# Performance work log

Hardware: AMD Instinct MI355X
Metric: run time of the kernel (lower is better)

Reference implementation:

```python
import math
import jax, jax.numpy as jnp
import numpy as np

H = 768      # hidden_size
NH = 12      # num_attention_heads
K = 3        # attention_num branches (wid = None, 2, 4)
DIV = 5.0    # gauss_divisor = 2**(attention_num-1) + 1
SFT = 1.0    # sft_factor
WIDTHS = (None, 2.0, 4.0)
B, L = 4, 1024


def _layernorm(x, s, b, eps=1e-5):
    m = jnp.mean(x, axis=-1, keepdims=True)
    v = jnp.mean((x - m) ** 2, axis=-1, keepdims=True)
    return (x - m) / jnp.sqrt(v + eps) * s + b


def _log_gauss_bias(props_len, width):
    # matches generate_gauss_weight + log(clamp_min(1e-6))
    center = jnp.arange(props_len, dtype=jnp.float32) / props_len          # (L,)
    wt = jnp.maximum(jnp.float32(width), 0.01) / DIV                       # scalar
    pos = jnp.linspace(0.0, 1.0, props_len)                                # (L,)
    g = (0.3989422804014327 / wt) * jnp.exp(-(pos[None, :] - center[:, None]) ** 2 / (2.0 * wt * wt))
    g = g / jnp.max(g, axis=-1, keepdims=True)
    return jnp.log(jnp.maximum(g, 1e-6))                                   # (L, L)


def _attn(qx, kx, vx, Wq, bq, Wk, bk, Wv, bv, bias, mask):
    Bn, Lq, D = qx.shape
    dh = D // NH
    q = (qx @ Wq + bq).reshape(Bn, Lq, NH, dh)
    k = (kx @ Wk + bk).reshape(Bn, kx.shape[1], NH, dh)
    v = (vx @ Wv + bv).reshape(Bn, vx.shape[1], NH, dh)
    s = jnp.einsum('bqhd,bkhd->bhqk', q, k) / math.sqrt(dh)
    if bias is not None:
        s = s + bias[None, None]                  # cached Gaussian log-bias
    if mask is not None:
        s = s + (1.0 - mask)[:, None, None, :] * (-10000.0)
    p = jax.nn.softmax(s, axis=-1)
    return jnp.einsum('bhqk,bkhd->bqhd', p, v).reshape(Bn, Lq, D)


def _block(x, mask, Wq, bq, Wk, bk, Wv, bv, W1, b1, W2, b2, n1s, n1b, n2s, n2b, bias):
    a = _attn(x, x, x, Wq, bq, Wk, bk, Wv, bv, bias, mask)
    x = _layernorm(x + a, n1s, n1b)
    h = jax.nn.relu(x @ W1 + b1) @ W2 + b2
    return _layernorm(x + h, n2s, n2b)


def setup_inputs():
    key = jax.random.key(0)
    ks = iter(jax.random.split(key, 64))
    def p(*sh):
        return jax.random.normal(next(ks), sh, dtype=jnp.float32) * 0.02
    inp = {}
    inp['input_tensor'] = jax.random.normal(next(ks), (B, L, H), dtype=jnp.float32)
    inp['attention_mask'] = jnp.ones((B, L), dtype=jnp.float32)
    for nm, sh in [('bWq', (K, H, H)), ('bWk', (K, H, H)), ('bWv', (K, H, H)),
                   ('bW1', (K, H, 4 * H)), ('bW2', (K, 4 * H, H)),
                   ('caWq', (H, H)), ('caWk', (H, H)), ('caWv', (H, H)),
                   ('caW1', (H, H)), ('caW2', (H, H)), ('Wl1', (H, H)), ('Wl2', (H, 1))]:
        inp[nm] = p(*sh)
    for nm, sh in [('bbq', (K, H)), ('bbk', (K, H)), ('bbv', (K, H)), ('bb1', (K, 4 * H)), ('bb2', (K, H)),
                   ('cabq', (H,)), ('cabk', (H,)), ('cabv', (H,)), ('cab1', (H,)), ('cab2', (H,)),
                   ('bl1', (H,)), ('bl2', (1,))]:
        inp[nm] = jnp.zeros(sh, dtype=jnp.float32)
    for nm, sh in [('bn1s', (K, H)), ('bn2s', (K, H)), ('bns', (H,)), ('can1s', (H,)), ('can2s', (H,))]:
        inp[nm] = jnp.ones(sh, dtype=jnp.float32)
    for nm, sh in [('bn1b', (K, H)), ('bn2b', (K, H)), ('bnb', (H,)), ('can1b', (H,)), ('can2b', (H,))]:
        inp[nm] = jnp.zeros(sh, dtype=jnp.float32)
    return inp


def reference(input_tensor, attention_mask, bWq, bbq, bWk, bbk, bWv, bbv, bW1, bb1, bW2, bb2,
              bn1s, bn1b, bn2s, bn2b, bns, bnb,
              caWq, cabq, caWk, cabk, caWv, cabv, caW1, cab1, caW2, cab2,
              can1s, can1b, can2s, can2b, Wl1, bl1, Wl2, bl2):
    Bn, Ln, _ = input_tensor.shape
    mask = attention_mask
    biases = [None if w is None else _log_gauss_bias(Ln, w) for w in WIDTHS]
    outs = []
    for i in range(K):
        o = _block(input_tensor, mask,
                   bWq[i], bbq[i], bWk[i], bbk[i], bWv[i], bbv[i],
                   bW1[i], bb1[i], bW2[i], bb2[i],
                   bn1s[i], bn1b[i], bn2s[i], bn2b[i], biases[i])
        outs.append(_layernorm(o, bns, bnb))
    oo = jnp.stack(outs, axis=-1)                                   # (B, L, H, K)
    valid = mask                                                    # (B, L)
    denom = jnp.maximum(valid.sum(axis=1, keepdims=True), 1.0)      # (B, 1)
    mean_token = (oo.mean(-1) * valid[:, :, None]).sum(axis=1, keepdims=True) / denom[:, :, None]  # (B,1,H)
    selected = mean_token  # weight_token=None, mode='global' -> global_token = mean_token
    branch_feat = jnp.transpose(oo, (0, 3, 1, 2)).reshape(Bn * K, Ln, H)
    query_token = jnp.repeat(selected, K, axis=0)                   # (B*K, 1, H)
    branch_mask = jnp.repeat(mask, K, axis=0)                       # (B*K, L)
    # CrossAttention (wid=None, FFN d_ff = H)
    a = _attn(query_token, branch_feat, branch_feat, caWq, cabq, caWk, cabk, caWv, cabv, None, branch_mask)
    q = _layernorm(query_token + a, can1s, can1b)
    t = jax.nn.relu(q @ caW1 + cab1) @ caW2 + cab2
    q = _layernorm(q + t, can2s, can2b)                             # (B*K, 1, H)
    w = q.reshape(Bn, K, H)
    w = jax.nn.relu(w @ Wl1 + bl1)
    w = (w @ Wl2 + bl2)[..., 0]                                     # (B, K)
    w = jax.nn.softmax(w / SFT, axis=-1)
    return (oo * w[:, None, None, :]).sum(axis=-1)                  # (B, L, H)
```

## Files before the change

### kernel.cpp

```cpp
#include <hip/hip_runtime.h>
#include <hip/hip_bf16.h>
#include <cstdint>
#include <cmath>

typedef __hip_bfloat16 bf16;
typedef __attribute__((ext_vector_type(8))) __bf16 bf16x8;
typedef __attribute__((ext_vector_type(4))) float f32x4;

#define NE2C ((size_t)4096 * 768)
#define WSQC ((size_t)768 * 768)

__device__ inline float ldv(const void* __restrict__ p, size_t i, bool b){
  return b ? __bfloat162float(((const bf16*)p)[i]) : ((const float*)p)[i];
}

__device__ inline float wave_sum(float v){
  #pragma unroll
  for (int o = 1; o < 64; o <<= 1) v += __shfl_xor(v, o, 64);
  return v;
}
__device__ inline float wave_max(float v){
  #pragma unroll
  for (int o = 1; o < 64; o <<= 1) v = fmaxf(v, __shfl_xor(v, o, 64));
  return v;
}

__device__ __forceinline__ void gload_lds16(const __bf16* g, __bf16* l){
  __builtin_amdgcn_global_load_lds(
      (const __attribute__((address_space(1))) uint32_t*)g,
      (__attribute__((address_space(3))) uint32_t*)l,
      16, 0, 0);
}

__global__ __launch_bounds__(256) void flagmask_kernel(const void* __restrict__ bns,
    const void* __restrict__ mask, int* __restrict__ flagp){
  const bool isb = (((const uint32_t*)bns)[0] != 0x3F800000u);
  int t = threadIdx.x;
  int ok = 1;
  for (int j = t; j < 4096; j += 256) ok &= (ldv(mask, (size_t)j, isb) == 1.0f) ? 1 : 0;
  __shared__ int allok;
  if (t == 0) { allok = 1; flagp[0] = isb ? 1 : 0; }
  __syncthreads();
  if (!ok) atomicAnd(&allok, 0);
  __syncthreads();
  if (t == 0) flagp[1] = allok;
}

__global__ __launch_bounds__(256) void cvtb_kernel(const void* __restrict__ in, __bf16* __restrict__ out,
                                                   int n, const int* __restrict__ flagp){
  const bool isb = flagp[0] != 0;
  int i = blockIdx.x * 256 + threadIdx.x;
  if (i < n) out[i] = (__bf16)ldv(in, i, isb);
}

__global__ __launch_bounds__(256) void transpose_kernel(const void* __restrict__ in, size_t in_off, size_t in_zstride,
    __bf16* __restrict__ out, size_t out_off, size_t out_zstride, int K, int N, const int* __restrict__ flagp)
{
  const bool isb = flagp[0] != 0;
  const int z = blockIdx.z;
  const size_t ioff = in_off + (size_t)z * in_zstride;
  __bf16* op = out + out_off + (size_t)z * out_zstride;
  const int n0 = blockIdx.x * 64, k0 = blockIdx.y * 64;
  __shared__ __bf16 T[64][65];
  const int cr = threadIdx.x >> 6, cc = threadIdx.x & 63;
  #pragma unroll
  for (int it = 0; it < 16; ++it) {
    int r = it * 4 + cr;
    T[r][cc] = (__bf16)ldv(in, ioff + (size_t)(k0 + r) * N + (n0 + cc), isb);
  }
  __syncthreads();
  #pragma unroll
  for (int it = 0; it < 16; ++it) {
    int r = it * 4 + cr;
    op[(size_t)(n0 + r) * K + (k0 + cc)] = T[cc][r];
  }
}

__global__ __launch_bounds__(256) void wqkvtrans_kernel(const void* __restrict__ bWq,
    const void* __restrict__ bWk, const void* __restrict__ bWv,
    __bf16* __restrict__ out, const int* __restrict__ flagp)
{
  const bool isb = flagp[0] != 0;
  const int z = blockIdx.z;
  const int br = z / 3, m = z % 3;
  const void* in = (m == 0) ? bWq : ((m == 1) ? bWk : bWv);
  const size_t ioff = (size_t)br * WSQC;
  __bf16* op = out + (size_t)z * WSQC;
  const int n0 = blockIdx.x * 64, k0 = blockIdx.y * 64;
  __shared__ __bf16 T[64][65];
  const int cr = threadIdx.x >> 6, cc = threadIdx.x & 63;
  #pragma unroll
  for (int it = 0; it < 16; ++it) {
    int r = it * 4 + cr;
    T[r][cc] = (__bf16)ldv(in, ioff + (size_t)(k0 + r) * 768 + (n0 + cc), isb);
  }
  __syncthreads();
  #pragma unroll
  for (int it = 0; it < 16; ++it) {
    int r = it * 4 + cr;
    op[(size_t)(n0 + r) * 768 + (k0 + cc)] = T[cc][r];
  }
}

__global__ __launch_bounds__(256) void vtrans_kernel(const __bf16* __restrict__ Rb, __bf16* __restrict__ VT)
{
  const int z = blockIdx.z;
  const int br = z >> 2, b = z & 3;
  const __bf16* src = Rb + (size_t)(br * 3 + 2) * NE2C;
  __bf16* dst = VT + (size_t)z * 786432;
  const int c0 = blockIdx.x * 64, k0 = blockIdx.y * 64;
  __shared__ __bf16 T[64][65];
  const int cr = threadIdx.x >> 6, cc = threadIdx.x & 63;
  #pragma unroll
  for (int it = 0; it < 16; ++it) {
    int k = it * 4 + cr;
    T[k][cc] = src[((size_t)(b * 1024 + k0 + k)) * 768 + c0 + cc];
  }
  __syncthreads();
  #pragma unroll
  for (int it = 0; it < 16; ++it) {
    int c = it * 4 + cr;
    dst[(size_t)(c0 + c) * 1024 + k0 + cc] = T[cc][c];
  }
}

__global__ __launch_bounds__(256) void biaspack_kernel(const void* bbq, const void* bbk, const void* bbv,
    const void* bb1, const void* bb2, const void* cabk, const void* cabv,
    float* __restrict__ pool, const int* __restrict__ flagp)
{
  const bool isb = flagp[0] != 0;
  int idx = blockIdx.x * 256 + threadIdx.x;
  if (idx >= 19968) return;
  float v;
  if (idx < 6912) {
    int i = idx / 2304, rem = idx % 2304;
    int m = rem / 768, c = rem % 768;
    const void* src = (m == 0) ? bbq : ((m == 1) ? bbk : bbv);
    v = ldv(src, (size_t)i * 768 + c, isb);
  } else if (idx < 16128) v = ldv(bb1, idx - 6912, isb);
  else if (idx < 18432)   v = ldv(bb2, idx - 16128, isb);
  else if (idx < 19200)   v = ldv(cabk, idx - 18432, isb);
  else                    v = ldv(cabv, idx - 19200, isb);
  pool[idx] = v;
}

__global__ __launch_bounds__(256) void gaussbias_kernel(float* __restrict__ gb)
{
  const int br = blockIdx.x >> 10;
  const int q  = blockIdx.x & 1023;
  const float inv2wt2 = (br == 0) ? 3.125f : 0.78125f;
  const float c2 = inv2wt2 * 1.4426950408889634f;
  const float cq = (float)q * (1.f / 1024.f);
  const float kst = roundf(cq * 1023.f);
  const float dd = kst * (1.f / 1023.f) - cq;
  const float dmin = dd * dd;
  float* row = gb + (size_t)br * 1048576 + (size_t)q * 1024;
  for (int o = threadIdx.x; o < 1024; o += 256) {
    int cb = o >> 6, rem = o & 63, rr = rem >> 2, t = rem & 3;
    int k = cb * 64 + t * 16 + rr;
    float d2 = (float)k * (1.f / 1023.f) - cq;
    row[o] = fmaxf((dmin - d2 * d2) * c2, -19.9315686f);
  }
}

template<int TAG>
__global__ __launch_bounds__(256) void gemm_mfma_kernel(
    const __bf16* __restrict__ A, size_t a_zstride,
    const __bf16* __restrict__ WT, const float* __restrict__ biasp,
    __bf16* __restrict__ C, int M, int N, int K, int relu)
{
  const int gx = gridDim.x, gy = gridDim.y;
  const int tot = gx * gy * gridDim.z;
  int p = (blockIdx.z * gy + blockIdx.y) * gx + blockIdx.x;
  int wg = (p & 7) * (tot >> 3) + (p >> 3);
  const int z = wg / (gx * gy);
  int rem = wg - z * gx * gy;
  const int m0 = (rem / gx) * 128, n0 = (rem % gx) * 128;

  A  += (size_t)z * a_zstride;
  WT += (size_t)z * (size_t)N * K;
  biasp += (size_t)z * N;
  C  += (size_t)z * (size_t)M * N;
  const int tid = threadIdx.x, w = tid >> 6, lane = tid & 63;
  const int quad = lane >> 4, r16 = lane & 15;
  const int wr = w >> 1, wc = w & 1;
  __shared__ __align__(16) __bf16 As[128 * 32];
  __shared__ __align__(16) __bf16 Bs[128 * 32];
  f32x4 acc[4][4];
  #pragma unroll
  for (int i = 0; i < 4; ++i)
    #pragma unroll
    for (int j = 0; j < 4; ++j) acc[i][j] = (f32x4){0.f, 0.f, 0.f, 0.f};

  const int srow = tid >> 2;
  const int scc  = (tid & 3) * 8;

  for (int k0 = 0; k0 < K; k0 += 32) {
    __syncthreads();
    #pragma unroll
    for (int it = 0; it < 2; ++it) {
      int row = it * 64 + srow;
      const __bf16* gA = A  + (size_t)(m0 + row) * K + k0 + scc;
      const __bf16* gB = WT + (size_t)(n0 + row) * K + k0 + scc;
      __bf16* lA = &As[(it * 256 + w * 64) * 8];
      __bf16* lB = &Bs[(it * 256 + w * 64) * 8];
      gload_lds16(gA, lA);
      gload_lds16(gB, lB);
    }
    __syncthreads();
    bf16x8 af[4], bf[4];
    #pragma unroll
    for (int mt = 0; mt < 4; ++mt) af[mt] = *(const bf16x8*)&As[(wr * 64 + mt * 16 + r16) * 32 + quad * 8];
    #pragma unroll
    for (int nt = 0; nt < 4; ++nt) bf[nt] = *(const bf16x8*)&Bs[(wc * 64 + nt * 16 + r16) * 32 + quad * 8];
    #pragma unroll
    for (int mt = 0; mt < 4; ++mt)
      #pragma unroll
      for (int nt = 0; nt < 4; ++nt)
        acc[mt][nt] = __builtin_amdgcn_mfma_f32_16x16x32_bf16(af[mt], bf[nt], acc[mt][nt], 0, 0, 0);
  }
  #pragma unroll
  for (int nt = 0; nt < 4; ++nt) {
    int col = n0 + wc * 64 + nt * 16 + r16;
    float bv = biasp[col];
    #pragma unroll
    for (int mt = 0; mt < 4; ++mt) {
      int rowb = m0 + wr * 64 + mt * 16 + quad * 4;
      #pragma unroll
      for (int reg = 0; reg < 4; ++reg) {
        float v = acc[mt][nt][reg] + bv;
        if (relu) v = fmaxf(v, 0.f);
        C[(size_t)(rowb + reg) * N + col] = (__bf16)v;
      }
    }
  }
}

__global__ __launch_bounds__(256) void gemm_ffn2_kernel(
    const __bf16* __restrict__ Hb, const __bf16* __restrict__ WT2,
    const float* __restrict__ biasp, __bf16* __restrict__ C0, __bf16* __restrict__ C1)
{
  const int gx = gridDim.x, gy = gridDim.y;
  const int tot = gx * gy * gridDim.z;
  int p = (blockIdx.z * gy + blockIdx.y) * gx + blockIdx.x;
  int wg = (p & 7) * (tot >> 3) + (p >> 3);
  const int z = wg / (gx * gy);
  int rem = wg - z * gx * gy;
  const int m0 = (rem / gx) * 128, n0 = (rem % gx) * 128;

  const int brn = z >> 1, half = z & 1;
  const __bf16* A  = Hb  + (size_t)brn * 4 * NE2C + half * 1536;
  const __bf16* WT = WT2 + (size_t)brn * 768 * 3072 + half * 1536;
  const float* bp = biasp + (size_t)brn * 768;
  __bf16* C = (half ? C1 : C0) + (size_t)brn * NE2C;
  const int tid = threadIdx.x, w = tid >> 6, lane = tid & 63;
  const int quad = lane >> 4, r16 = lane & 15;
  const int wr = w >> 1, wc = w & 1;
  __shared__ __align__(16) __bf16 As[128 * 32];
  __shared__ __align__(16) __bf16 Bs[128 * 32];
  f32x4 acc[4][4];
  #pragma unroll
  for (int i = 0; i < 4; ++i)
    #pragma unroll
    for (int j = 0; j < 4; ++j) acc[i][j] = (f32x4){0.f, 0.f, 0.f, 0.f};

  const int srow = tid >> 2;
  const int scc  = (tid & 3) * 8;

  for (int k0 = 0; k0 < 1536; k0 += 32) {
    __syncthreads();
    #pragma unroll
    for (int it = 0; it < 2; ++it) {
      int row = it * 64 + srow;
      const __bf16* gA = A  + (size_t)(m0 + row) * 3072 + k0 + scc;
      const __bf16* gB = WT + (size_t)(n0 + row) * 3072 + k0 + scc;
      gload_lds16(gA, &As[(it * 256 + w * 64) * 8]);
      gload_lds16(gB, &Bs[(it * 256 + w * 64) * 8]);
    }
    __syncthreads();
    bf16x8 af[4], bf[4];
    #pragma unroll
    for (int mt = 0; mt < 4; ++mt) af[mt] = *(const bf16x8*)&As[(wr * 64 + mt * 16 + r16) * 32 + quad * 8];
    #pragma unroll
    for (int nt = 0; nt < 4; ++nt) bf[nt] = *(const bf16x8*)&Bs[(wc * 64 + nt * 16 + r16) * 32 + quad * 8];
    #pragma unroll
    for (int mt = 0; mt < 4; ++mt)
      #pragma unroll
      for (int nt = 0; nt < 4; ++nt)
        acc[mt][nt] = __builtin_amdgcn_mfma_f32_16x16x32_bf16(af[mt], bf[nt], acc[mt][nt], 0, 0, 0);
  }
  #pragma unroll
  for (int nt = 0; nt < 4; ++nt) {
    int col = n0 + wc * 64 + nt * 16 + r16;
    float bv = half ? 0.f : bp[col];
    #pragma unroll
    for (int mt = 0; mt < 4; ++mt) {
      int rowb = m0 + wr * 64 + mt * 16 + quad * 4;
      #pragma unroll
      for (int reg = 0; reg < 4; ++reg)
        C[(size_t)(rowb + reg) * 768 + col] = (__bf16)(acc[mt][nt][reg] + bv);
    }
  }
}

__global__ __launch_bounds__(256) void gemm_small_kernel(const float* __restrict__ A, const void* __restrict__ W,
    size_t woff, const void* __restrict__ bias, size_t boff, float* __restrict__ C,
    int N, int K, int relu, const int* __restrict__ flagp)
{
  const bool isb = flagp[0] != 0;
  const int row = blockIdx.y;
  const int c = blockIdx.x * 64 + (threadIdx.x & 63);
  const int ks = threadIdx.x >> 6;
  const int klen = K >> 2;
  const float* ar = A + (size_t)row * K + ks * klen;
  const size_t wbase = woff + (size_t)ks * klen * N + c;
  float acc = 0.f;
  #pragma unroll 4
  for (int k = 0; k < klen; ++k)
    acc += ar[k] * ldv(W, wbase + (size_t)k * N, isb);
  __shared__ float red[4][64];
  red[ks][threadIdx.x & 63] = acc;
  __syncthreads();
  if (threadIdx.x < 64) {
    float v = red[0][threadIdx.x] + red[1][threadIdx.x] + red[2][threadIdx.x] + red[3][threadIdx.x];
    v += ldv(bias, boff + c, isb);
    if (relu) v = fmaxf(v, 0.f);
    C[(size_t)row * N + c] = v;
  }
}

__global__ __launch_bounds__(512) void attn_mfma_kernel(
    const __bf16* __restrict__ QKV, const void* __restrict__ mask,
    const float* __restrict__ gbias,
    __bf16* __restrict__ Aout, const int* __restrict__ flagp)
{
  const bool isb = flagp[0] != 0;
  const bool mall = flagp[1] != 0;
  const int gx = gridDim.x, gy = gridDim.y;
  const int tot = gx * gy * gridDim.z;
  int p = (blockIdx.z * gy + blockIdx.y) * gx + blockIdx.x;
  int wg = (p & 7) * (tot >> 3) + (p >> 3);
  const int bz = wg / (gx * gy);
  int rem2 = wg - bz * gx * gy;
  const int h = rem2 / gx;
  const int qblk = rem2 % gx;

  const int b = bz & 3, br = bz >> 2;
  const __bf16* Q  = QKV + (size_t)br * 3 * NE2C;
  const __bf16* Kg = Q + NE2C;
  const __bf16* VgT = QKV + 9 * NE2C + (size_t)bz * 786432;
  Aout += (size_t)br * NE2C;
  const int has_bias = br > 0;

  const int tid = threadIdx.x;
  const int w = tid >> 6, lane = tid & 63;
  const int quad = lane >> 4, r16 = lane & 15;
  const int qbase = qblk * 128 + w * 16;

  __shared__ __align__(16) __bf16 Ks[64 * 72];
  __shared__ __align__(16) __bf16 Vt[64 * 72];
  __shared__ __align__(16) __bf16 Ps[8][16 * 72];

  const __bf16* qrow = Q + ((size_t)(b * 1024 + qbase + r16)) * 768 + h * 64;
  bf16x8 aq0 = *(const bf16x8*)(qrow + quad * 8);
  bf16x8 aq1 = *(const bf16x8*)(qrow + 32 + quad * 8);

  const float* bq4[4];
  if (has_bias) {
    const float* gbb = gbias + (size_t)(br - 1) * 1048576 + r16 * 4;
    #pragma unroll
    for (int reg = 0; reg < 4; ++reg)
      bq4[reg] = gbb + (size_t)(qbase + quad * 4 + reg) * 1024;
  }

  float m_r[4], l_r[4];
  f32x4 O[4];
  #pragma unroll
  for (int n = 0; n < 4; ++n) O[n] = (f32x4){0.f, 0.f, 0.f, 0.f};
  #pragma unroll
  for (int reg = 0; reg < 4; ++reg) { m_r[reg] = -1e30f; l_r[reg] = 0.f; }

  const int sr0  = tid >> 3;
  const int sc8  = (tid & 7) * 8;
  const size_t kcol  = (size_t)h * 64 + sc8;
  const size_t bbase = (size_t)b * 1024;
  const __bf16* vbase = VgT + (size_t)(h * 64 + sr0) * 1024 + sc8;
  const int vls = sr0 * 72 + (((sc8 >> 3) ^ ((sr0 >> 3) & 7)) * 8);

  const float SCL = 0.18033688f;
  const float MBIG = 14426.9504f;
  const float THR2 = 11.5415603f;

  bf16x8 kpre, vpre;
  kpre = *(const bf16x8*)(Kg + (bbase + sr0) * 768 + kcol);
  vpre = *(const bf16x8*)(vbase);

  for (int c0 = 0; c0 < 1024; c0 += 64) {
    __syncthreads();
    *(bf16x8*)&Ks[sr0 * 72 + sc8] = kpre;
    *(bf16x8*)&Vt[vls] = vpre;
    __syncthreads();

    if (c0 + 64 < 1024) {
      kpre = *(const bf16x8*)(Kg + (bbase + c0 + 64 + sr0) * 768 + kcol);
      vpre = *(const bf16x8*)(vbase + c0 + 64);
    }

    f32x4 bv4[4];
    if (has_bias) {
      #pragma unroll
      for (int reg = 0; reg < 4; ++reg) bv4[reg] = *(const f32x4*)(bq4[reg] + c0);
    }

    float s4[4][4], p4[4][4];
    #pragma unroll
    for (int t = 0; t < 4; ++t) {
      bf16x8 b0 = *(const bf16x8*)&Ks[(t * 16 + r16) * 72 + quad * 8];
      bf16x8 b1 = *(const bf16x8*)&Ks[(t * 16 + r16) * 72 + 32 + quad * 8];
      f32x4 accq = (f32x4){0.f, 0.f, 0.f, 0.f};
      accq = __builtin_amdgcn_mfma_f32_16x16x32_bf16(aq0, b0, accq, 0, 0, 0);
      accq = __builtin_amdgcn_mfma_f32_16x16x32_bf16(aq1, b1, accq, 0, 0, 0);
      float mterm = 0.f;
      if (!mall) {
        int kk = c0 + t * 16 + r16;
        float mk = ldv(mask, (size_t)(b * 1024 + kk), isb);
        mterm = fmaf(mk, MBIG, -MBIG);
      }
      if (has_bias) {
        #pragma unroll
        for (int reg = 0; reg < 4; ++reg)
          s4[t][reg] = fmaf(accq[reg], SCL, mterm) + bv4[reg][t];
      } else {
        #pragma unroll
        for (int reg = 0; reg < 4; ++reg)
          s4[t][reg] = fmaf(accq[reg], SCL, mterm);
      }
    }
    float mlane[4];
    #pragma unroll
    for (int reg = 0; reg < 4; ++reg)
      mlane[reg] = fmaxf(fmaxf(s4[0][reg], s4[1][reg]), fmaxf(s4[2][reg], s4[3][reg]));
    bool need = (mlane[0] > m_r[0] + THR2) || (mlane[1] > m_r[1] + THR2)
             || (mlane[2] > m_r[2] + THR2) || (mlane[3] > m_r[3] + THR2);
    if (__any(need)) {
      #pragma unroll
      for (int reg = 0; reg < 4; ++reg) {
        float t0 = mlane[reg];
        #pragma unroll
        for (int off = 1; off < 16; off <<= 1) t0 = fmaxf(t0, __shfl_xor(t0, off, 64));
        float mnew = fmaxf(m_r[reg], t0);
        float alpha = exp2f(m_r[reg] - mnew);
        l_r[reg] *= alpha;
        m_r[reg] = mnew;
        #pragma unroll
        for (int n = 0; n < 4; ++n) O[n][reg] *= alpha;
      }
    }
    #pragma unroll
    for (int reg = 0; reg < 4; ++reg) {
      float rs = 0.f;
      #pragma unroll
      for (int t = 0; t < 4; ++t) { float p2 = exp2f(s4[t][reg] - m_r[reg]); p4[t][reg] = p2; rs += p2; }
      l_r[reg] += rs;
    }
    __bf16* pw = &Ps[w][0];
    #pragma unroll
    for (int t = 0; t < 4; ++t)
      #pragma unroll
      for (int reg = 0; reg < 4; ++reg)
        pw[(quad * 4 + reg) * 72 + t * 16 + r16] = (__bf16)p4[t][reg];
    bf16x8 ap0 = *(const bf16x8*)&pw[r16 * 72 + quad * 8];
    bf16x8 ap1 = *(const bf16x8*)&pw[r16 * 72 + 32 + quad * 8];
    __builtin_amdgcn_s_setprio(1);
    #pragma unroll
    for (int n = 0; n < 4; ++n) {
      int dr = n * 16 + r16;
      int sw = (dr >> 3) & 7;
      bf16x8 bv0 = *(const bf16x8*)&Vt[dr * 72 + (quad ^ sw) * 8];
      bf16x8 bv1 = *(const bf16x8*)&Vt[dr * 72 + ((quad + 4) ^ sw) * 8];
      O[n] = __builtin_amdgcn_mfma_f32_16x16x32_bf16(ap0, bv0, O[n], 0, 0, 0);
      O[n] = __builtin_amdgcn_mfma_f32_16x16x32_bf16(ap1, bv1, O[n], 0, 0, 0);
    }
    __builtin_amdgcn_s_setprio(0);
  }
  #pragma unroll
  for (int reg = 0; reg < 4; ++reg) {
    float lv = l_r[reg];
    #pragma unroll
    for (int off = 1; off < 16; off <<= 1) lv += __shfl_xor(lv, off, 64);
    l_r[reg] = lv;
  }
  #pragma unroll
  for (int n = 0; n < 4; ++n)
    #pragma unroll
    for (int reg = 0; reg < 4; ++reg) {
      int qg = qbase + quad * 4 + reg;
      Aout[((size_t)(b * 1024 + qg)) * 768 + h * 64 + n * 16 + r16] = (__bf16)(O[n][reg] / l_r[reg]);
    }
}

__global__ __launch_bounds__(256) void lnb_b_kernel(const __bf16* __restrict__ x, const __bf16* __restrict__ a,
    const void* __restrict__ sc, const void* __restrict__ bi, __bf16* __restrict__ out,
    const int* __restrict__ flagp)
{
  const bool isb = flagp[0] != 0;
  const int br = blockIdx.y;
  a   += (size_t)br * NE2C;
  out += (size_t)br * NE2C;
  const size_t so = (size_t)br * 768;
  int r = blockIdx.x;
  const __bf16* xr = x + (size_t)r * 768;
  const __bf16* ar = a + (size_t)r * 768;
  int t = threadIdx.x;
  float v[3]; float s = 0.f, ss = 0.f;
  #pragma unroll
  for (int j = 0; j < 3; j++) {
    int c = t + j * 256;
    float val = (float)xr[c] + (float)ar[c];
    v[j] = val; s += val; ss += val * val;
  }
  s = wave_sum(s); ss = wave_sum(ss);
  __shared__ float sred[8];
  __shared__ float stats[2];
  int lane = t & 63, wid = t >> 6;
  if (lane == 0) { sred[wid] = s; sred[4 + wid] = ss; }
  __syncthreads();
  if (t == 0) {
    float S = sred[0] + sred[1] + sred[2] + sred[3];
    float SS = sred[4] + sred[5] + sred[6] + sred[7];
    float mean = S * (1.f / 768.f);
    float var = fmaxf(SS * (1.f / 768.f) - mean * mean, 0.f);
    stats[0] = mean; stats[1] = rsqrtf(var + 1e-5f);
  }
  __syncthreads();
  float mean = stats[0], rstd = stats[1];
  #pragma unroll
  for (int j = 0; j < 3; j++) {
    int c = t + j * 256;
    out[(size_t)r * 768 + c] = (__bf16)((v[j] - mean) * rstd * ldv(sc, so + c, isb) + ldv(bi, so + c, isb));
  }
}

__global__ __launch_bounds__(256) void lnb2_b_kernel(const __bf16* __restrict__ x, const __bf16* __restrict__ a,
    const __bf16* __restrict__ a2,
    const void* __restrict__ sc1, const void* __restrict__ bi1,
    const void* __restrict__ sc2, const void* __restrict__ bi2,
    __bf16* __restrict__ out, const int* __restrict__ flagp)
{
  const bool isb = flagp[0] != 0;
  const int br = blockIdx.y;
  x   += (size_t)br * NE2C;
  a   += (size_t)br * NE2C;
  a2  += (size_t)br * NE2C;
  out += (size_t)br * NE2C;
  const size_t s1off = (size_t)br * 768;
  int r = blockIdx.x;
  const __bf16* xr = x + (size_t)r * 768;
  const __bf16* ar = a + (size_t)r * 768;
  const __bf16* ar2 = a2 + (size_t)r * 768;
  int t = threadIdx.x;
  int lane = t & 63, wid = t >> 6;
  __shared__ float sred[8], stats[2], sred2[8], stats2[2];

  float v[3]; float s = 0.f, ss = 0.f;
  #pragma unroll
  for (int j = 0; j < 3; j++) {
    int c = t + j * 256;
    float val = (float)xr[c] + (float)ar[c] + (float)ar2[c];
    v[j] = val; s += val; ss += val * val;
  }
  s = wave_sum(s); ss = wave_sum(ss);
  if (lane == 0) { sred[wid] = s; sred[4 + wid] = ss; }
  __syncthreads();
  if (t == 0) {
    float S = sred[0] + sred[1] + sred[2] + sred[3];
    float SS = sred[4] + sred[5] + sred[6] + sred[7];
    float mean = S * (1.f / 768.f);
    float var = fmaxf(SS * (1.f / 768.f) - mean * mean, 0.f);
    stats[0] = mean; stats[1] = rsqrtf(var + 1e-5f);
  }
  __syncthreads();
  float mean = stats[0], rstd = stats[1];
  float y[3]; float s2 = 0.f, ss2 = 0.f;
  #pragma unroll
  for (int j = 0; j < 3; j++) {
    int c = t + j * 256;
    float yv = (v[j] - mean) * rstd * ldv(sc1, s1off + c, isb) + ldv(bi1, s1off + c, isb);
    yv = (float)(__bf16)yv;
    y[j] = yv; s2 += yv; ss2 += yv * yv;
  }
  s2 = wave_sum(s2); ss2 = wave_sum(ss2);
  if (lane == 0) { sred2[wid] = s2; sred2[4 + wid] = ss2; }
  __syncthreads();
  if (t == 0) {
    float S = sred2[0] + sred2[1] + sred2[2] + sred2[3];
    float SS = sred2[4] + sred2[5] + sred2[6] + sred2[7];
    float mean2 = S * (1.f / 768.f);
    float var2 = fmaxf(SS * (1.f / 768.f) - mean2 * mean2, 0.f);
    stats2[0] = mean2; stats2[1] = rsqrtf(var2 + 1e-5f);
  }
  __syncthreads();
  float mean2 = stats2[0], rstd2 = stats2[1];
  #pragma unroll
  for (int j = 0; j < 3; j++) {
    int c = t + j * 256;
    out[(size_t)r * 768 + c] = (__bf16)((y[j] - mean2) * rstd2 * ldv(sc2, c, isb) + ldv(bi2, c, isb));
  }
}

__global__ __launch_bounds__(256) void ln_kernel(const float* __restrict__ x, const float* __restrict__ a,
    const void* __restrict__ sc, size_t soff, const void* __restrict__ bi, size_t boff,
    float* __restrict__ out, int xdiv, const int* __restrict__ flagp)
{
  const bool isb = flagp[0] != 0;
  int r = blockIdx.x;
  const float* xr = x + (size_t)(xdiv > 1 ? r / xdiv : r) * 768;
  const float* ar = a ? a + (size_t)r * 768 : nullptr;
  int t = threadIdx.x;
  float v[3]; float s = 0.f, ss = 0.f;
  #pragma unroll
  for (int j = 0; j < 3; j++) {
    int c = t + j * 256;
    float val = xr[c] + (ar ? ar[c] : 0.f);
    v[j] = val; s += val; ss += val * val;
  }
  s = wave_sum(s); ss = wave_sum(ss);
  __shared__ float sred[8];
  __shared__ float stats[2];
  int lane = t & 63, wid = t >> 6;
  if (lane == 0) { sred[wid] = s; sred[4 + wid] = ss; }
  __syncthreads();
  if (t == 0) {
    float S = sred[0] + sred[1] + sred[2] + sred[3];
    float SS = sred[4] + sred[5] + sred[6] + sred[7];
    float mean = S * (1.f / 768.f);
    float var = fmaxf(SS * (1.f / 768.f) - mean * mean, 0.f);
    stats[0] = mean; stats[1] = rsqrtf(var + 1e-5f);
  }
  __syncthreads();
  float mean = stats[0], rstd = stats[1];
  #pragma unroll
  for (int j = 0; j < 3; j++) {
    int c = t + j * 256;
    out[(size_t)r * 768 + c] = (v[j] - mean) * rstd * ldv(sc, soff + c, isb) + ldv(bi, boff + c, isb);
  }
}

__global__ __launch_bounds__(256) void meantok_part_kernel(const __bf16* __restrict__ OO, const void* __restrict__ mask,
    float* __restrict__ partials, const int* __restrict__ flagp)
{
  const bool isb = flagp[0] != 0;
  const size_t NE = NE2C;
  int h = blockIdx.x * 256 + threadIdx.x;
  int b = blockIdx.y, lc = blockIdx.z;
  const __bf16* base = OO + (size_t)(b * 1024 + lc * 16) * 768 + h;
  float acc = 0.f;
  for (int l = 0; l < 16; ++l) {
    float mk = ldv(mask, (size_t)(b * 1024 + lc * 16 + l), isb);
    size_t off = (size_t)l * 768;
    acc += mk * ((float)base[off] + (float)base[off + NE] + (float)base[off + 2 * NE]);
  }
  partials[((size_t)(b * 64 + lc)) * 768 + h] = acc;
}

__global__ __launch_bounds__(256) void meantok_fin_kernel(const float* __restrict__ partials,
    const void* __restrict__ mask, float* __restrict__ mt, const int* __restrict__ flagp)
{
  const bool isb = flagp[0] != 0;
  int h = blockIdx.x * 256 + threadIdx.x;
  int b = blockIdx.y;
  int t = threadIdx.x;
  float ms = 0.f;
  for (int j = t; j < 1024; j += 256) ms += ldv(mask, (size_t)(b * 1024 + j), isb);
  ms = wave_sum(ms);
  __shared__ float sred[4];
  __shared__ float msume;
  if ((t & 63) == 0) sred[t >> 6] = ms;
  __syncthreads();
  if (t == 0) msume = fmaxf(sred[0] + sred[1] + sred[2] + sred[3], 1.f);
  __syncthreads();
  float acc = 0.f;
  #pragma unroll
  for (int lc = 0; lc < 64; ++lc) acc += partials[((size_t)(b * 64 + lc)) * 768 + h];
  mt[b * 768 + h] = acc * (1.f / 3.f) / msume;
}

__global__ __launch_bounds__(256) void crossattn_kernel(const float* __restrict__ qC, const __bf16* __restrict__ kC,
    const __bf16* __restrict__ vC, const void* __restrict__ mask, float* __restrict__ caout,
    const int* __restrict__ flagp)
{
  const bool isb = flagp[0] != 0;
  const bool mall = flagp[1] != 0;
  int h = blockIdx.x, i = blockIdx.y, b = blockIdx.z;
  int tid = threadIdx.x, lane = tid & 63, wv = tid >> 6;
  __shared__ float sbuf[1024];
  __shared__ float qsh[64];
  __shared__ float red[8];
  __shared__ float vred[4][64];
  if (tid < 64) qsh[tid] = qC[b * 768 + h * 64 + tid];
  __syncthreads();
  const size_t rowbase = (size_t)(i * 4 + b) * 1024;
  const __bf16* kb = kC + rowbase * 768 + h * 64;
  float lmax = -1e30f;
  for (int j = tid; j < 1024; j += 256) {
    const __bf16* kr = kb + (size_t)j * 768;
    float s = 0.f;
    #pragma unroll
    for (int d0 = 0; d0 < 8; ++d0) {
      bf16x8 kv = *(const bf16x8*)(kr + d0 * 8);
      #pragma unroll
      for (int e = 0; e < 8; ++e) s += qsh[d0 * 8 + e] * (float)kv[e];
    }
    s *= 0.125f;
    if (!mall) {
      float mk = ldv(mask, (size_t)(b * 1024 + j), isb);
      s += (1.0f - mk) * (-10000.0f);
    }
    sbuf[j] = s;
    lmax = fmaxf(lmax, s);
  }
  lmax = wave_max(lmax);
  if (lane == 0) red[wv] = lmax;
  __syncthreads();
  float mm = fmaxf(fmaxf(red[0], red[1]), fmaxf(red[2], red[3]));
  float lsum = 0.f;
  for (int j = tid; j < 1024; j += 256) {
    float p = __expf(sbuf[j] - mm);
    sbuf[j] = p;
    lsum += p;
  }
  lsum = wave_sum(lsum);
  if (lane == 0) red[4 + wv] = lsum;
  __syncthreads();
  float L = red[4] + red[5] + red[6] + red[7];
  const __bf16* vb = vC + rowbase * 768 + h * 64;
  float acc = 0.f;
  for (int j = wv * 256; j < wv * 256 + 256; ++j)
    acc += sbuf[j] * (float)vb[(size_t)j * 768 + lane];
  vred[wv][lane] = acc;
  __syncthreads();
  if (tid < 64) {
    float a = vred[0][tid] + vred[1][tid] + vred[2][tid] + vred[3][tid];
    caout[(size_t)(b * 3 + i) * 768 + h * 64 + tid] = a / L;
  }
}

__global__ __launch_bounds__(256) void logits_kernel(const float* __restrict__ wfeat, const void* __restrict__ Wl2,
    const void* __restrict__ bl2, float* __restrict__ logits, const int* __restrict__ flagp)
{
  const bool isb = flagp[0] != 0;
  int r = blockIdx.x, t = threadIdx.x;
  float s = 0.f;
  #pragma unroll
  for (int j = 0; j < 3; j++) {
    int c = t + j * 256;
    s += wfeat[(size_t)r * 768 + c] * ldv(Wl2, c, isb);
  }
  s = wave_sum(s);
  __shared__ float sred[4];
  if ((t & 63) == 0) sred[t >> 6] = s;
  __syncthreads();
  if (t == 0) logits[r] = sred[0] + sred[1] + sred[2] + sred[3] + ldv(bl2, 0, isb);
}

__global__ void wsoftmax_kernel(const float* __restrict__ logits, float* __restrict__ w)
{
  int b = threadIdx.x;
  if (b < 4) {
    float l0 = logits[b * 3], l1 = logits[b * 3 + 1], l2 = logits[b * 3 + 2];
    float m = fmaxf(l0, fmaxf(l1, l2));
    float e0 = __expf(l0 - m), e1 = __expf(l1 - m), e2 = __expf(l2 - m);
    float inv = 1.f / (e0 + e1 + e2);
    w[b * 3] = e0 * inv; w[b * 3 + 1] = e1 * inv; w[b * 3 + 2] = e2 * inv;
  }
}

__global__ __launch_bounds__(256) void combine_kernel(const __bf16* __restrict__ OO, const float* __restrict__ w,
                                                      void* __restrict__ out, const int* __restrict__ flagp)
{
  const bool isb = flagp[0] != 0;
  const size_t NE = NE2C;
  size_t idx = (size_t)blockIdx.x * 256 + threadIdx.x;
  int b = (int)(idx / (1024 * 768));
  float w0 = w[b * 3], w1 = w[b * 3 + 1], w2 = w[b * 3 + 2];
  float v = (float)OO[idx] * w0 + (float)OO[idx + NE] * w1 + (float)OO[idx + 2 * NE] * w2;
  if (isb) ((bf16*)out)[idx] = __float2bfloat16(v);
  else     ((float*)out)[idx] = v;
}

extern "C" void kernel_launch(void* const* d_in, const int* in_sizes, int n_in,
                              void* d_out, int out_size, void* d_ws, size_t ws_size,
                              hipStream_t stream)
{
  const void* X    = d_in[0];
  const void* mask = d_in[1];
  const void* bWq  = d_in[2];
  const void* bWk  = d_in[3];
  const void* bWv  = d_in[4];
  const void* bW1  = d_in[5];
  const void* bW2  = d_in[6];
  const void* caWq = d_in[7];
  const void* caWk = d_in[8];
  const void* caWv = d_in[9];
  const void* caW1 = d_in[10];
  const void* caW2 = d_in[11];
  const void* Wl1  = d_in[12];
  const void* Wl2  = d_in[13];
  const void* bbq  = d_in[14];
  const void* bbk  = d_in[15];
  const void* bbv  = d_in[16];
  const void* bb1  = d_in[17];
  const void* bb2  = d_in[18];
  const void* cabq = d_in[19];
  const void* cabk = d_in[20];
  const void* cabv = d_in[21];
  const void* cab1 = d_in[22];
  const void* cab2 = d_in[23];
  const void* bl1  = d_in[24];
  const void* bl2  = d_in[25];
  const void* bn1s = d_in[26];
  const void* bn2s = d_in[27];
  const void* bns  = d_in[28];
  const void* can1s= d_in[29];
  const void* can2s= d_in[30];
  const void* bn1b = d_in[31];
  const void* bn2b = d_in[32];
  const void* bnb  = d_in[33];
  const void* can1b= d_in[34];
  const void* can2b= d_in[35];

  const size_t NE2 = NE2C;
  const size_t WSQ = WSQC;
  const size_t WSF = (size_t)768 * 3072;

  __bf16* XFb  = (__bf16*)d_ws;
  __bf16* Rb   = XFb + NE2;
  __bf16* X1   = Rb + 12 * NE2;
  __bf16* AF2  = X1 + 3 * NE2;
  __bf16* WTqkv= AF2 + 3 * NE2;
  __bf16* WT1  = WTqkv + 9 * WSQ;
  __bf16* WT2  = WT1 + 3 * WSF;
  __bf16* WTc  = WT2 + 3 * WSF;
  float*  pool = (float*)(WTc + 2 * WSQ);
  float*  mt     = pool + 19968;
  float*  qC     = mt + 3072;
  float*  caout  = qC + 3072;
  float*  q1     = caout + 9216;
  float*  t1     = q1 + 9216;
  float*  t2     = t1 + 9216;
  float*  q2     = t2 + 9216;
  float*  wfeat  = q2 + 9216;
  float*  logits = wfeat + 9216;
  float*  wsm    = logits + 16;
  int*    flagp  = (int*)(wsm + 16);
  __bf16* OO = X1;
  __bf16* kC = Rb;
  __bf16* vC = Rb + 3 * NE2;
  __bf16* VT = Rb + 9 * NE2;
  float*  gb = (float*)X1;
  float*  partials = (float*)AF2;
  __bf16* F2b = WTqkv;

  dim3 blk256(256);
  flagmask_kernel<<<dim3(1), blk256, 0, stream>>>(bns, mask, flagp);
  cvtb_kernel<<<dim3((int)((NE2 + 255) / 256)), blk256, 0, stream>>>(X, XFb, (int)NE2, flagp);

  wqkvtrans_kernel<<<dim3(12, 12, 9), blk256, 0, stream>>>(bWq, bWk, bWv, WTqkv, flagp);
  transpose_kernel<<<dim3(48, 12, 3), blk256, 0, stream>>>(bW1, 0, WSF, WT1, 0, WSF, 768, 3072, flagp);
  transpose_kernel<<<dim3(12, 48, 3), blk256, 0, stream>>>(bW2, 0, WSF, WT2, 0, WSF, 3072, 768, flagp);
  transpose_kernel<<<dim3(12, 12, 1), blk256, 0, stream>>>(caWk, 0, 0, WTc, 0, 0, 768, 768, flagp);
  transpose_kernel<<<dim3(12, 12, 1), blk256, 0, stream>>>(caWv, 0, 0, WTc, WSQ, 0, 768, 768, flagp);
  biaspack_kernel<<<dim3(78), blk256, 0, stream>>>(bbq, bbk, bbv, bb1, bb2, cabk, cabv, pool, flagp);
  gaussbias_kernel<<<dim3(2048), blk256, 0, stream>>>(gb);

  gemm_mfma_kernel<0><<<dim3(6, 32, 9), blk256, 0, stream>>>(XFb, 0, WTqkv, pool, Rb, 4096, 768, 768, 0);
  vtrans_kernel<<<dim3(12, 16, 12), blk256, 0, stream>>>(Rb, VT);
  attn_mfma_kernel<<<dim3(8, 12, 12), dim3(512), 0, stream>>>(Rb, mask, gb, AF2, flagp);
  lnb_b_kernel<<<dim3(4096, 3), blk256, 0, stream>>>(XFb, AF2, bn1s, bn1b, X1, flagp);
  gemm_mfma_kernel<1><<<dim3(24, 32, 3), blk256, 0, stream>>>(X1, NE2, WT1, pool + 6912, Rb, 4096, 3072, 768, 1);
  gemm_ffn2_kernel<<<dim3(6, 32, 6), blk256, 0, stream>>>(Rb, WT2, pool + 16128, AF2, F2b);
  lnb2_b_kernel<<<dim3(4096, 3), blk256, 0, stream>>>(X1, AF2, F2b, bn2s, bn2b, bns, bnb, OO, flagp);

  meantok_part_kernel<<<dim3(3, 4, 64), blk256, 0, stream>>>(OO, mask, partials, flagp);
  meantok_fin_kernel<<<dim3(3, 4), blk256, 0, stream>>>(partials, mask, mt, flagp);
  gemm_small_kernel<<<dim3(12, 4), blk256, 0, stream>>>(mt, caWq, 0, cabq, 0, qC, 768, 768, 0, flagp);
  gemm_mfma_kernel<3><<<dim3(6, 96, 2), blk256, 0, stream>>>(OO, 0, WTc, pool + 18432, kC, 12288, 768, 768, 0);
  crossattn_kernel<<<dim3(12, 3, 4), blk256, 0, stream>>>(qC, kC, vC, mask, caout, flagp);
  ln_kernel<<<dim3(12), blk256, 0, stream>>>(mt, caout, can1s, 0, can1b, 0, q1, 3, flagp);
  gemm_small_kernel<<<dim3(12, 12), blk256, 0, stream>>>(q1, caW1, 0, cab1, 0, t1, 768, 768, 1, flagp);
  gemm_small_kernel<<<dim3(12, 12), blk256, 0, stream>>>(t1, caW2, 0, cab2, 0, t2, 768, 768, 0, flagp);
  ln_kernel<<<dim3(12), blk256, 0, stream>>>(q1, t2, can2s, 0, can2b, 0, q2, 1, flagp);
  gemm_small_kernel<<<dim3(12, 12), blk256, 0, stream>>>(q2, Wl1, 0, bl1, 0, wfeat, 768, 768, 1, flagp);
  logits_kernel<<<dim3(12), blk256, 0, stream>>>(wfeat, Wl2, bl2, logits, flagp);
  wsoftmax_kernel<<<dim3(1), dim3(64), 0, stream>>>(logits, wsm);
  combine_kernel<<<dim3((int)(NE2 / 256)), blk256, 0, stream>>>(OO, wsm, d_out, flagp);
}
```

Before: 864.2 us.

## Fuse cross-attention tail (LN, FFN, LN, linear, logits) into one kernel

Replaces six small launches (two layernorms, three small GEMVs, logits reduction) with a single 12-block kernel that keeps intermediates in shared memory. This removes launch overhead and global round-trips for the tiny per-row tail. In exchange, each block streams three full 768x768 weight matrices by itself with only 12 blocks active, so per-kernel parallelism drops sharply compared with the previous 144-block GEMVs.

Result: slower. 1.264 ms (+46.2%).

```diff
diff --git a/kernel.cpp b/kernel.cpp
--- a/kernel.cpp
+++ b/kernel.cpp
@@ -326,6 +326,139 @@
     v += ldv(bias, boff + c, isb);
     if (relu) v = fmaxf(v, 0.f);
     C[(size_t)row * N + c] = v;
+  }
+}
+
+__global__ __launch_bounds__(256) void tailfuse_kernel(
+    const float* __restrict__ mt, const float* __restrict__ caout,
+    const void* __restrict__ can1s, const void* __restrict__ can1b,
+    const void* __restrict__ can2s, const void* __restrict__ can2b,
+    const void* __restrict__ caW1, const void* __restrict__ cab1,
+    const void* __restrict__ caW2, const void* __restrict__ cab2,
+    const void* __restrict__ Wl1, const void* __restrict__ bl1,
+    const void* __restrict__ Wl2, const void* __restrict__ bl2,
+    float* __restrict__ logits, const int* __restrict__ flagp)
+{
+  const bool isb = flagp[0] != 0;
+  const int r = blockIdx.x;
+  const int t = threadIdx.x;
+  const int lane = t & 63, wid = t >> 6;
+  __shared__ float q1s[768], bufs[768];
+  __shared__ float sred[8], stats[2];
+
+  const float* xr = mt + (size_t)(r / 3) * 768;
+  const float* ar = caout + (size_t)r * 768;
+  {
+    float v[3]; float s = 0.f, ss = 0.f;
+    #pragma unroll
+    for (int j = 0; j < 3; ++j) {
+      int c = t + j * 256;
+      float val = xr[c] + ar[c];
+      v[j] = val; s += val; ss += val * val;
+    }
+    s = wave_sum(s); ss = wave_sum(ss);
+    if (lane == 0) { sred[wid] = s; sred[4 + wid] = ss; }
+    __syncthreads();
+    if (t == 0) {
+      float S = sred[0] + sred[1] + sred[2] + sred[3];
+      float SS = sred[4] + sred[5] + sred[6] + sred[7];
+      float mean = S * (1.f / 768.f);
+      float var = fmaxf(SS * (1.f / 768.f) - mean * mean, 0.f);
+      stats[0] = mean; stats[1] = rsqrtf(var + 1e-5f);
+    }
+    __syncthreads();
+    float mean = stats[0], rstd = stats[1];
+    #pragma unroll
+    for (int j = 0; j < 3; ++j) {
+      int c = t + j * 256;
+      q1s[c] = (v[j] - mean) * rstd * ldv(can1s, c, isb) + ldv(can1b, c, isb);
+    }
+  }
+  __syncthreads();
+
+  {
+    float acc0 = 0.f, acc1 = 0.f, acc2 = 0.f;
+    #pragma unroll 4
+    for (int k = 0; k < 768; ++k) {
+      float qv = q1s[k];
+      size_t base = (size_t)k * 768 + t;
+      acc0 += qv * ldv(caW1, base, isb);
+      acc1 += qv * ldv(caW1, base + 256, isb);
+      acc2 += qv * ldv(caW1, base + 512, isb);
+    }
+    __syncthreads();
+    bufs[t]       = fmaxf(acc0 + ldv(cab1, t, isb), 0.f);
+    bufs[t + 256] = fmaxf(acc1 + ldv(cab1, t + 256, isb), 0.f);
+    bufs[t + 512] = fmaxf(acc2 + ldv(cab1, t + 512, isb), 0.f);
+  }
+  __syncthreads();
+
+  float y[3];
+  {
+    float acc0 = 0.f, acc1 = 0.f, acc2 = 0.f;
+    #pragma unroll 4
+    for (int k = 0; k < 768; ++k) {
+      float tv = bufs[k];
+      size_t base = (size_t)k * 768 + t;
+      acc0 += tv * ldv(caW2, base, isb);
+      acc1 += tv * ldv(caW2, base + 256, isb);
+      acc2 += tv * ldv(caW2, base + 512, isb);
+    }
+    float s = 0.f, ss = 0.f;
+    y[0] = q1s[t]       + acc0 + ldv(cab2, t, isb);
+    y[1] = q1s[t + 256] + acc1 + ldv(cab2, t + 256, isb);
+    y[2] = q1s[t + 512] + acc2 + ldv(cab2, t + 512, isb);
+    #pragma unroll
+    for (int j = 0; j < 3; ++j) { s += y[j]; ss += y[j] * y[j]; }
+    s = wave_sum(s); ss = wave_sum(ss);
+    __syncthreads();
+    if (lane == 0) { sred[wid] = s; sred[4 + wid] = ss; }
+    __syncthreads();
+    if (t == 0) {
+      float S = sred[0] + sred[1] + sred[2] + sred[3];
+      float SS = sred[4] + sred[5] + sred[6] + sred[7];
+      float mean = S * (1.f / 768.f);
+      float var = fmaxf(SS * (1.f / 768.f) - mean * mean, 0.f);
+      stats[0] = mean; stats[1] = rsqrtf(var + 1e-5f);
+    }
+    __syncthreads();
+    float mean = stats[0], rstd = stats[1];
+    #pragma unroll
+    for (int j = 0; j < 3; ++j) {
+      int c = t + j * 256;
+      bufs[c] = (y[j] - mean) * rstd * ldv(can2s, c, isb) + ldv(can2b, c, isb);
+    }
+  }
+  __syncthreads();
+
+  {
+    float acc0 = 0.f, acc1 = 0.f, acc2 = 0.f;
+    #pragma unroll 4
+    for (int k = 0; k < 768; ++k) {
+      float qv = bufs[k];
+      size_t base = (size_t)k * 768 + t;
+      acc0 += qv * ldv(Wl1, base, isb);
+      acc1 += qv * ldv(Wl1, base + 256, isb);
+      acc2 += qv * ldv(Wl1, base + 512, isb);
+    }
+    __syncthreads();
+    q1s[t]       = fmaxf(acc0 + ldv(bl1, t, isb), 0.f);
+    q1s[t + 256] = fmaxf(acc1 + ldv(bl1, t + 256, isb), 0.f);
+    q1s[t + 512] = fmaxf(acc2 + ldv(bl1, t + 512, isb), 0.f);
+  }
+  __syncthreads();
+
+  {
+    float s = 0.f;
+    #pragma unroll
+    for (int j = 0; j < 3; ++j) {
+      int c = t + j * 256;
+      s += q1s[c] * ldv(Wl2, c, isb);
+    }
+    s = wave_sum(s);
+    if (lane == 0) sred[wid] = s;
+    __syncthreads();
+    if (t == 0) logits[r] = sred[0] + sred[1] + sred[2] + sred[3] + ldv(bl2, 0, isb);
   }
 }
 
@@ -608,44 +741,6 @@
   }
 }
 
-__global__ __launch_bounds__(256) void ln_kernel(const float* __restrict__ x, const float* __restrict__ a,
-    const void* __restrict__ sc, size_t soff, const void* __restrict__ bi, size_t boff,
-    float* __restrict__ out, int xdiv, const int* __restrict__ flagp)
-{
-  const bool isb = flagp[0] != 0;
-  int r = blockIdx.x;
-  const float* xr = x + (size_t)(xdiv > 1 ? r / xdiv : r) * 768;
-  const float* ar = a ? a + (size_t)r * 768 : nullptr;
-  int t = threadIdx.x;
-  float v[3]; float s = 0.f, ss = 0.f;
-  #pragma unroll
-  for (int j = 0; j < 3; j++) {
-    int c = t + j * 256;
-    float val = xr[c] + (ar ? ar[c] : 0.f);
-    v[j] = val; s += val; ss += val * val;
-  }
-  s = wave_sum(s); ss = wave_sum(ss);
-  __shared__ float sred[8];
-  __shared__ float stats[2];
-  int lane = t & 63, wid = t >> 6;
-  if (lane == 0) { sred[wid] = s; sred[4 + wid] = ss; }
-  __syncthreads();
-  if (t == 0) {
-    float S = sred[0] + sred[1] + sred[2] + sred[3];
-    float SS = sred[4] + sred[5] + sred[6] + sred[7];
-    float mean = S * (1.f / 768.f);
-    float var = fmaxf(SS * (1.f / 768.f) - mean * mean, 0.f);
-    stats[0] = mean; stats[1] = rsqrtf(var + 1e-5f);
-  }
-  __syncthreads();
-  float mean = stats[0], rstd = stats[1];
-  #pragma unroll
-  for (int j = 0; j < 3; j++) {
-    int c = t + j * 256;
-    out[(size_t)r * 768 + c] = (v[j] - mean) * rstd * ldv(sc, soff + c, isb) + ldv(bi, boff + c, isb);
-  }
-}
-
 __global__ __launch_bounds__(256) void meantok_part_kernel(const __bf16* __restrict__ OO, const void* __restrict__ mask,
     float* __restrict__ partials, const int* __restrict__ flagp)
 {
@@ -743,24 +838,6 @@
     float a = vred[0][tid] + vred[1][tid] + vred[2][tid] + vred[3][tid];
     caout[(size_t)(b * 3 + i) * 768 + h * 64 + tid] = a / L;
   }
-}
-
-__global__ __launch_bounds__(256) void logits_kernel(const float* __restrict__ wfeat, const void* __restrict__ Wl2,
-    const void* __restrict__ bl2, float* __restrict__ logits, const int* __restrict__ flagp)
-{
-  const bool isb = flagp[0] != 0;
-  int r = blockIdx.x, t = threadIdx.x;
-  float s = 0.f;
-  #pragma unroll
-  for (int j = 0; j < 3; j++) {
-    int c = t + j * 256;
-    s += wfeat[(size_t)r * 768 + c] * ldv(Wl2, c, isb);
-  }
-  s = wave_sum(s);
-  __shared__ float sred[4];
-  if ((t & 63) == 0) sred[t >> 6] = s;
-  __syncthreads();
-  if (t == 0) logits[r] = sred[0] + sred[1] + sred[2] + sred[3] + ldv(bl2, 0, isb);
 }
 
 __global__ void wsoftmax_kernel(const float* __restrict__ logits, float* __restrict__ w)
@@ -845,12 +922,7 @@
   float*  mt     = pool + 19968;
   float*  qC     = mt + 3072;
   float*  caout  = qC + 3072;
-  float*  q1     = caout + 9216;
-  float*  t1     = q1 + 9216;
-  float*  t2     = t1 + 9216;
-  float*  q2     = t2 + 9216;
-  float*  wfeat  = q2 + 9216;
-  float*  logits = wfeat + 9216;
+  float*  logits = caout + 9216;
   float*  wsm    = logits + 16;
   int*    flagp  = (int*)(wsm + 16);
   __bf16* OO = X1;
@@ -886,12 +958,8 @@
   gemm_small_kernel<<<dim3(12, 4), blk256, 0, stream>>>(mt, caWq, 0, cabq, 0, qC, 768, 768, 0, flagp);
   gemm_mfma_kernel<3><<<dim3(6, 96, 2), blk256, 0, stream>>>(OO, 0, WTc, pool + 18432, kC, 12288, 768, 768, 0);
   crossattn_kernel<<<dim3(12, 3, 4), blk256, 0, stream>>>(qC, kC, vC, mask, caout, flagp);
-  ln_kernel<<<dim3(12), blk256, 0, stream>>>(mt, caout, can1s, 0, can1b, 0, q1, 3, flagp);
-  gemm_small_kernel<<<dim3(12, 12), blk256, 0, stream>>>(q1, caW1, 0, cab1, 0, t1, 768, 768, 1, flagp);
-  gemm_small_kernel<<<dim3(12, 12), blk256, 0, stream>>>(t1, caW2, 0, cab2, 0, t2, 768, 768, 0, flagp);
-  ln_kernel<<<dim3(12), blk256, 0, stream>>>(q1, t2, can2s, 0, can2b, 0, q2, 1, flagp);
-  gemm_small_kernel<<<dim3(12, 12), blk256, 0, stream>>>(q2, Wl1, 0, bl1, 0, wfeat, 768, 768, 1, flagp);
-  logits_kernel<<<dim3(12), blk256, 0, stream>>>(wfeat, Wl2, bl2, logits, flagp);
+  tailfuse_kernel<<<dim3(12), blk256, 0, stream>>>(mt, caout, can1s, can1b, can2s, can2b,
+      caW1, cab1, caW2, cab2, Wl1, bl1, Wl2, bl2, logits, flagp);
   wsoftmax_kernel<<<dim3(1), dim3(64), 0, stream>>>(logits, wsm);
   combine_kernel<<<dim3((int)(NE2 / 256)), blk256, 0, stream>>>(OO, wsm, d_out, flagp);
 }
```
